# Performance work log

Hardware: AMD Instinct MI355X
Metric: run time of the kernel (lower is better)

## Reference

```python
import jax, jax.numpy as jnp
import numpy as np

B, IN, OUT = 8192, 1024, 1024


def setup_inputs() -> dict:
    key = jax.random.key(0)
    k1, k2 = jax.random.split(key)
    x = jax.random.normal(k1, (B, IN), dtype=jnp.float32)
    W_seed = jax.random.normal(k2, (IN, OUT), dtype=jnp.float32) / np.sqrt(IN).astype(np.float32)
    b_seed = jnp.zeros((OUT,), dtype=jnp.float32)
    W_sig = jnp.zeros((2,), dtype=jnp.float32)  # mixture logits over ['dense','Toeplitz']
    b_sig = jnp.zeros((2,), dtype=jnp.float32)  # mixture logits over ['dense','None']
    A_sig = jnp.zeros((2,), dtype=jnp.float32)  # mixture logits over ['linear','relu']
    return {"x": x, "W_seed": W_seed, "b_seed": b_seed,
            "W_sig": W_sig, "b_sig": b_sig, "A_sig": A_sig}


def _toeplitz_from_seed(W_seed):
    # seed_vec = [W_seed[0, out-1], ..., W_seed[0, 1], W_seed[0,0], ..., W_seed[in-1,0]]
    in_sz, out_sz = W_seed.shape
    seed_vec = jnp.concatenate([W_seed[0, -1:0:-1], W_seed[:, 0]])  # [out-1 + in]
    # W_toep[i, j] = seed_vec[i - j + out - 1]
    idx = jnp.arange(in_sz)[:, None] - jnp.arange(out_sz)[None, :] + (out_sz - 1)
    return seed_vec[idx]  # [in, out]


def reference(x, W_seed, b_seed, W_sig, b_sig, A_sig):
    W_toep = _toeplitz_from_seed(W_seed)
    w_s = jax.nn.softmax(W_sig)
    W_core = w_s[0] * W_seed + w_s[1] * W_toep          # softmax-weighted weight mixture
    b_s = jax.nn.softmax(b_sig)
    b_core = b_s[0] * b_seed                             # 'None' branch contributes zeros
    out = x @ W_core + b_core                            # [B, out]
    a_s = jax.nn.softmax(A_sig)
    return a_s[0] * out + a_s[1] * jax.nn.relu(out)      # activation mixture
```

## Files before the change

### kernel.cpp

```cpp
#include <hip/hip_runtime.h>

typedef unsigned short ushort_t;
typedef __bf16 bf16x8 __attribute__((ext_vector_type(8)));
typedef float f32x4 __attribute__((ext_vector_type(4)));

#define AS1 __attribute__((address_space(1)))
#define AS3 __attribute__((address_space(3)))

__device__ __forceinline__ ushort_t f2bf(float f) {
    unsigned u = __builtin_bit_cast(unsigned, f);
    u = (u + 0x7fffu + ((u >> 16) & 1u)) >> 16;
    return (ushort_t)u;
}

__device__ __forceinline__ void async16(void* lds, const void* g) {
    __builtin_amdgcn_global_load_lds((const AS1 unsigned int*)g,
                                     (AS3 unsigned int*)lds, 16, 0, 0);
}

__device__ __forceinline__ void softmax2(const float* __restrict__ sig, float& s0, float& s1) {
    float a = sig[0], b = sig[1];
    float m = fmaxf(a, b);
    float e0 = __expf(a - m), e1 = __expf(b - m);
    float inv = 1.0f / (e0 + e1);
    s0 = e0 * inv; s1 = e1 * inv;
}

__device__ __forceinline__ float toep_val(const float* __restrict__ Wseed, int k, int o) {
    return (k >= o) ? Wseed[(size_t)(k - o) << 10] : Wseed[o - k];
}

__global__ __launch_bounds__(256) void prep_kernel(const float* __restrict__ x,
                                                   const float* __restrict__ Wseed,
                                                   const float* __restrict__ Wsig,
                                                   ushort_t* __restrict__ xb,
                                                   ushort_t* __restrict__ Wt) {
    int b = blockIdx.x;
    if (b < 4096) {
        int i = b * 256 + threadIdx.x;
        const float4* xp = (const float4*)x + (size_t)i * 2;
        float4 a = xp[0], c = xp[1];
        uint4 r;
        r.x = (unsigned)f2bf(a.x) | ((unsigned)f2bf(a.y) << 16);
        r.y = (unsigned)f2bf(a.z) | ((unsigned)f2bf(a.w) << 16);
        r.z = (unsigned)f2bf(c.x) | ((unsigned)f2bf(c.y) << 16);
        r.w = (unsigned)f2bf(c.z) | ((unsigned)f2bf(c.w) << 16);
        ((uint4*)xb)[i] = r;
        return;
    }
    __shared__ float T[64][65];
    int bb = b - 4096;
    int k0 = (bb >> 4) * 64;
    int o0 = (bb & 15) * 64;
    int t = threadIdx.x;
    #pragma unroll
    for (int i = 0; i < 4; ++i) {
        int lin = t + i * 256;
        int kr = lin >> 4;
        int c4 = lin & 15;
        float4 v = *(const float4*)&Wseed[(size_t)(k0 + kr) * 1024 + o0 + c4 * 4];
        T[kr][c4 * 4 + 0] = v.x;
        T[kr][c4 * 4 + 1] = v.y;
        T[kr][c4 * 4 + 2] = v.z;
        T[kr][c4 * 4 + 3] = v.w;
    }
    __syncthreads();
    float s0, s1; softmax2(Wsig, s0, s1);
    #pragma unroll
    for (int i = 0; i < 2; ++i) {
        int lin = t + i * 256;
        int oo = lin >> 3;
        int kq = (lin & 7) * 8;
        unsigned r[4];
        #pragma unroll
        for (int q = 0; q < 4; ++q) {
            float v0 = s0 * T[kq + 2 * q + 0][oo] + s1 * toep_val(Wseed, k0 + kq + 2 * q + 0, o0 + oo);
            float v1 = s0 * T[kq + 2 * q + 1][oo] + s1 * toep_val(Wseed, k0 + kq + 2 * q + 1, o0 + oo);
            r[q] = (unsigned)f2bf(v0) | ((unsigned)f2bf(v1) << 16);
        }
        *(uint4*)&Wt[(size_t)(o0 + oo) * 1024 + k0 + kq] = make_uint4(r[0], r[1], r[2], r[3]);
    }
}

#define BM 128
#define BN 128
#define BK 64
#define NKT 16

__global__ __launch_bounds__(256, 2) void gemm_kernel(const ushort_t* __restrict__ Xb,
                                                      const ushort_t* __restrict__ Wt,
                                                      const float* __restrict__ bseed,
                                                      const float* __restrict__ bsig,
                                                      const float* __restrict__ asig,
                                                      float* __restrict__ out) {
    __shared__ ushort_t lds[32768];
    ushort_t* At0 = lds;
    ushort_t* Bt0 = lds + 8192;
    ushort_t* At1 = lds + 16384;
    ushort_t* Bt1 = lds + 24576;

    const int t = threadIdx.x;
    const int wv = t >> 6;
    const int lane = t & 63;

    const int orig = blockIdx.x;
    const int g = orig & 7;
    const int within = orig >> 3;
    const int rb = g * 8 + (within >> 3);
    const int cb = within & 7;
    const int brow = rb * BM;
    const int bcol = cb * BN;

    const int rs = t >> 3;
    const int cs = (t & 7) ^ (rs & 7);
    const ushort_t* gA = Xb + (size_t)(brow + rs) * 1024 + 8 * cs;
    const ushort_t* gB = Wt + (size_t)(bcol + rs) * 1024 + 8 * cs;

    f32x4 acc[4][4];
    #pragma unroll
    for (int i = 0; i < 4; ++i)
        #pragma unroll
        for (int j = 0; j < 4; ++j) acc[i][j] = (f32x4){0.f, 0.f, 0.f, 0.f};

    const int wr = (wv >> 1) * 64;
    const int wcn = (wv & 1) * 64;
    const int fr = lane & 15;
    const int kq = lane >> 4;

    float bs0, bs1, as0, as1;
    softmax2(bsig, bs0, bs1);
    softmax2(asig, as0, as1);
    float bias[4];
    #pragma unroll
    for (int ni = 0; ni < 4; ++ni)
        bias[ni] = bs0 * bseed[bcol + wcn + ni * 16 + fr];
    asm volatile("" :: "v"(bias[0]), "v"(bias[1]), "v"(bias[2]), "v"(bias[3]),
                       "v"(as0), "v"(as1));
    asm volatile("" ::: "memory");

#define STAGE1(buf, gptr, ko)                                      \
    do {                                                           \
        async16((buf) + wv * 512,        (gptr) + (ko));           \
        async16((buf) + 2048 + wv * 512, (gptr) + 32768 + (ko));   \
        async16((buf) + 4096 + wv * 512, (gptr) + 65536 + (ko));   \
        async16((buf) + 6144 + wv * 512, (gptr) + 98304 + (ko));   \
    } while (0)

#define STAGE(Abuf, Bbuf, ko) do { STAGE1(Abuf, gA, ko); STAGE1(Bbuf, gB, ko); } while (0)

#define COMPUTE(Abuf, Bbuf)                                                        \
    do {                                                                           \
        bf16x8 af[4][2], bf[4][2];                                                 \
        _Pragma("unroll")                                                          \
        for (int mi = 0; mi < 4; ++mi) {                                           \
            int row_ = wr + mi * 16 + fr;                                          \
            af[mi][0] = *(const bf16x8*)&(Abuf)[row_ * 64 + (((kq)     ^ (row_ & 7)) << 3)]; \
            af[mi][1] = *(const bf16x8*)&(Abuf)[row_ * 64 + (((kq + 4) ^ (row_ & 7)) << 3)]; \
        }                                                                          \
        _Pragma("unroll")                                                          \
        for (int ni = 0; ni < 4; ++ni) {                                           \
            int row_ = wcn + ni * 16 + fr;                                         \
            bf[ni][0] = *(const bf16x8*)&(Bbuf)[row_ * 64 + (((kq)     ^ (row_ & 7)) << 3)]; \
            bf[ni][1] = *(const bf16x8*)&(Bbuf)[row_ * 64 + (((kq + 4) ^ (row_ & 7)) << 3)]; \
        }                                                                          \
        _Pragma("unroll")                                                          \
        for (int mi = 0; mi < 4; ++mi)                                             \
            _Pragma("unroll")                                                      \
            for (int ni = 0; ni < 4; ++ni) {                                       \
                acc[mi][ni] = __builtin_amdgcn_mfma_f32_16x16x32_bf16(             \
                    af[mi][0], bf[ni][0], acc[mi][ni], 0, 0, 0);                   \
                acc[mi][ni] = __builtin_amdgcn_mfma_f32_16x16x32_bf16(             \
                    af[mi][1], bf[ni][1], acc[mi][ni], 0, 0, 0);                   \
            }                                                                      \
    } while (0)

#define SYNC() do { asm volatile("s_waitcnt vmcnt(0) lgkmcnt(0)" ::: "memory");    \
                    __builtin_amdgcn_s_barrier(); } while (0)

    STAGE(At0, Bt0, 0);
    SYNC();
    for (int it = 0; it < 7; ++it) {
        STAGE(At1, Bt1, (2 * it + 1) * BK);
        COMPUTE(At0, Bt0);
        SYNC();
        STAGE(At0, Bt0, (2 * it + 2) * BK);
        COMPUTE(At1, Bt1);
        SYNC();
    }
    STAGE(At1, Bt1, 15 * BK);
    COMPUTE(At0, Bt0);
    SYNC();
    COMPUTE(At1, Bt1);

    #pragma unroll
    for (int ni = 0; ni < 4; ++ni) {
        int col = bcol + wcn + ni * 16 + fr;
        #pragma unroll
        for (int mi = 0; mi < 4; ++mi) {
            int row = brow + wr + mi * 16 + (lane >> 4) * 4;
            #pragma unroll
            for (int r = 0; r < 4; ++r) {
                float v = acc[mi][ni][r] + bias[ni];
                out[(size_t)(row + r) * 1024 + col] = as0 * v + as1 * fmaxf(v, 0.f);
            }
        }
    }
#undef STAGE1
#undef STAGE
#undef COMPUTE
#undef SYNC
}

__global__ __launch_bounds__(256) void naive_kernel(const float* __restrict__ x,
                                                    const float* __restrict__ Wseed,
                                                    const float* __restrict__ bseed,
                                                    const float* __restrict__ Wsig,
                                                    const float* __restrict__ bsig,
                                                    const float* __restrict__ asig,
                                                    float* __restrict__ out) {
    int idx = blockIdx.x * 256 + threadIdx.x;
    int b = idx >> 10, o = idx & 1023;
    float ws0, ws1, bs0, bs1, as0, as1;
    softmax2(Wsig, ws0, ws1);
    softmax2(bsig, bs0, bs1);
    softmax2(asig, as0, as1);
    float s = 0.f;
    const float* xr = x + (size_t)b * 1024;
    for (int k = 0; k < 1024; ++k) {
        float wc = ws0 * Wseed[((size_t)k << 10) + o] + ws1 * toep_val(Wseed, k, o);
        s += xr[k] * wc;
    }
    float v = s + bs0 * bseed[o];
    out[idx] = as0 * v + as1 * fmaxf(v, 0.f);
}

extern "C" void kernel_launch(void* const* d_in, const int* in_sizes, int n_in,
                              void* d_out, int out_size, void* d_ws, size_t ws_size,
                              hipStream_t stream) {
    const float* x     = (const float*)d_in[0];
    const float* Wseed = (const float*)d_in[1];
    const float* bseed = (const float*)d_in[2];
    const float* Wsig  = (const float*)d_in[3];
    const float* bsig  = (const float*)d_in[4];
    const float* Asig  = (const float*)d_in[5];
    float* out = (float*)d_out;

    const size_t need = (2u << 20) + (16u << 20) + 1024;
    if (ws_size < need) {
        naive_kernel<<<dim3(8192 * 1024 / 256), dim3(256), 0, stream>>>(
            x, Wseed, bseed, Wsig, bsig, Asig, out);
        return;
    }

    ushort_t* Wt = (ushort_t*)d_ws;
    ushort_t* Xb = (ushort_t*)((char*)d_ws + (2u << 20));

    prep_kernel<<<dim3(4096 + 256), dim3(256), 0, stream>>>(x, Wseed, Wsig, Xb, Wt);
    gemm_kernel<<<dim3(512), dim3(256), 0, stream>>>(Xb, Wt, bseed, bsig, Asig, out);
}
```

Before: 39.45 us.

## Fuse fp32-to-bf16 conversion of x into GEMM A-tile loading

Drops the separate x-to-bf16 conversion pass and its 16MB workspace round trip. The GEMM now loads fp32 x tiles into registers one stage ahead, converts them to bf16 and writes them into swizzled LDS, while W tiles still use async global-to-LDS loads. Partial vmcnt waits let the register prefetch overlap with compute. The cost is more global bytes per A tile, more VGPR pressure from 16 prefetched float4 registers, and conversion work inside the main loop.

```diff
diff --git a/kernel.cpp b/kernel.cpp
--- a/kernel.cpp
+++ b/kernel.cpp
@@ -30,26 +30,11 @@
     return (k >= o) ? Wseed[(size_t)(k - o) << 10] : Wseed[o - k];
 }
 
-__global__ __launch_bounds__(256) void prep_kernel(const float* __restrict__ x,
-                                                   const float* __restrict__ Wseed,
-                                                   const float* __restrict__ Wsig,
-                                                   ushort_t* __restrict__ xb,
-                                                   ushort_t* __restrict__ Wt) {
-    int b = blockIdx.x;
-    if (b < 4096) {
-        int i = b * 256 + threadIdx.x;
-        const float4* xp = (const float4*)x + (size_t)i * 2;
-        float4 a = xp[0], c = xp[1];
-        uint4 r;
-        r.x = (unsigned)f2bf(a.x) | ((unsigned)f2bf(a.y) << 16);
-        r.y = (unsigned)f2bf(a.z) | ((unsigned)f2bf(a.w) << 16);
-        r.z = (unsigned)f2bf(c.x) | ((unsigned)f2bf(c.y) << 16);
-        r.w = (unsigned)f2bf(c.z) | ((unsigned)f2bf(c.w) << 16);
-        ((uint4*)xb)[i] = r;
-        return;
-    }
+__global__ __launch_bounds__(256) void prep_w_kernel(const float* __restrict__ Wseed,
+                                                     const float* __restrict__ Wsig,
+                                                     ushort_t* __restrict__ Wt) {
     __shared__ float T[64][65];
-    int bb = b - 4096;
+    int bb = blockIdx.x;
     int k0 = (bb >> 4) * 64;
     int o0 = (bb & 15) * 64;
     int t = threadIdx.x;
@@ -87,17 +72,17 @@
 #define BK 64
 #define NKT 16
 
-__global__ __launch_bounds__(256, 2) void gemm_kernel(const ushort_t* __restrict__ Xb,
+__global__ __launch_bounds__(256, 2) void gemm_kernel(const float* __restrict__ Xf,
                                                       const ushort_t* __restrict__ Wt,
                                                       const float* __restrict__ bseed,
                                                       const float* __restrict__ bsig,
                                                       const float* __restrict__ asig,
                                                       float* __restrict__ out) {
     __shared__ ushort_t lds[32768];
-    ushort_t* At0 = lds;
-    ushort_t* Bt0 = lds + 8192;
-    ushort_t* At1 = lds + 16384;
-    ushort_t* Bt1 = lds + 24576;
+    ushort_t* const A0buf = lds;
+    ushort_t* const A1buf = lds + 8192;
+    ushort_t* const B0buf = lds + 16384;
+    ushort_t* const B1buf = lds + 24576;
 
     const int t = threadIdx.x;
     const int wv = t >> 6;
@@ -113,19 +98,21 @@
 
     const int rs = t >> 3;
     const int cs = (t & 7) ^ (rs & 7);
-    const ushort_t* gA = Xb + (size_t)(brow + rs) * 1024 + 8 * cs;
     const ushort_t* gB = Wt + (size_t)(bcol + rs) * 1024 + 8 * cs;
 
-    f32x4 acc[4][4];
-    #pragma unroll
-    for (int i = 0; i < 4; ++i)
-        #pragma unroll
-        for (int j = 0; j < 4; ++j) acc[i][j] = (f32x4){0.f, 0.f, 0.f, 0.f};
+    const float* gX = Xf + (size_t)(brow + (t >> 3)) * 1024 + (t & 7) * 8;
+    const int wbase = (t >> 3) * 64 + (((t & 7) ^ ((t >> 3) & 7)) << 3);
 
     const int wr = (wv >> 1) * 64;
     const int wcn = (wv & 1) * 64;
     const int fr = lane & 15;
     const int kq = lane >> 4;
+
+    f32x4 acc[4][4];
+    #pragma unroll
+    for (int i = 0; i < 4; ++i)
+        #pragma unroll
+        for (int j = 0; j < 4; ++j) acc[i][j] = (f32x4){0.f, 0.f, 0.f, 0.f};
 
     float bs0, bs1, as0, as1;
     softmax2(bsig, bs0, bs1);
@@ -138,15 +125,47 @@
                        "v"(as0), "v"(as1));
     asm volatile("" ::: "memory");
 
-#define STAGE1(buf, gptr, ko)                                      \
-    do {                                                           \
-        async16((buf) + wv * 512,        (gptr) + (ko));           \
-        async16((buf) + 2048 + wv * 512, (gptr) + 32768 + (ko));   \
-        async16((buf) + 4096 + wv * 512, (gptr) + 65536 + (ko));   \
-        async16((buf) + 6144 + wv * 512, (gptr) + 98304 + (ko));   \
-    } while (0)
-
-#define STAGE(Abuf, Bbuf, ko) do { STAGE1(Abuf, gA, ko); STAGE1(Bbuf, gB, ko); } while (0)
+    f32x4 aE0, aE1, aE2, aE3, aE4, aE5, aE6, aE7;
+    f32x4 aO0, aO1, aO2, aO3, aO4, aO5, aO6, aO7;
+
+#define LOADA(P, ko)                                                   \
+    do {                                                               \
+        P##0 = *(const f32x4*)(gX + (ko));                             \
+        P##1 = *(const f32x4*)(gX + (ko) + 4);                         \
+        P##2 = *(const f32x4*)(gX + 32768 + (ko));                     \
+        P##3 = *(const f32x4*)(gX + 32768 + (ko) + 4);                 \
+        P##4 = *(const f32x4*)(gX + 65536 + (ko));                     \
+        P##5 = *(const f32x4*)(gX + 65536 + (ko) + 4);                 \
+        P##6 = *(const f32x4*)(gX + 98304 + (ko));                     \
+        P##7 = *(const f32x4*)(gX + 98304 + (ko) + 4);                 \
+    } while (0)
+
+#define CVW(Abuf, off, rlo, rhi)                                       \
+    do {                                                               \
+        bf16x8 v_;                                                     \
+        _Pragma("unroll")                                              \
+        for (int j_ = 0; j_ < 4; ++j_) {                               \
+            v_[j_]     = (__bf16)rlo[j_];                              \
+            v_[4 + j_] = (__bf16)rhi[j_];                              \
+        }                                                              \
+        *(bf16x8*)&(Abuf)[(off)] = v_;                                 \
+    } while (0)
+
+#define WRITEA(Abuf, P)                                                \
+    do {                                                               \
+        CVW(Abuf, wbase,        P##0, P##1);                           \
+        CVW(Abuf, wbase + 2048, P##2, P##3);                           \
+        CVW(Abuf, wbase + 4096, P##4, P##5);                           \
+        CVW(Abuf, wbase + 6144, P##6, P##7);                           \
+    } while (0)
+
+#define STAGEB(buf, ko)                                                \
+    do {                                                               \
+        async16((buf) + wv * 512,        gB + (ko));                   \
+        async16((buf) + 2048 + wv * 512, gB + 32768 + (ko));           \
+        async16((buf) + 4096 + wv * 512, gB + 65536 + (ko));           \
+        async16((buf) + 6144 + wv * 512, gB + 98304 + (ko));           \
+    } while (0)
 
 #define COMPUTE(Abuf, Bbuf)                                                        \
     do {                                                                           \
@@ -174,23 +193,38 @@
             }                                                                      \
     } while (0)
 
-#define SYNC() do { asm volatile("s_waitcnt vmcnt(0) lgkmcnt(0)" ::: "memory");    \
-                    __builtin_amdgcn_s_barrier(); } while (0)
-
-    STAGE(At0, Bt0, 0);
-    SYNC();
-    for (int it = 0; it < 7; ++it) {
-        STAGE(At1, Bt1, (2 * it + 1) * BK);
-        COMPUTE(At0, Bt0);
-        SYNC();
-        STAGE(At0, Bt0, (2 * it + 2) * BK);
-        COMPUTE(At1, Bt1);
-        SYNC();
-    }
-    STAGE(At1, Bt1, 15 * BK);
-    COMPUTE(At0, Bt0);
-    SYNC();
-    COMPUTE(At1, Bt1);
+#define ENDSYNC8() do { asm volatile("" ::: "memory");                               \
+                        asm volatile("s_waitcnt vmcnt(8)" ::: "memory");             \
+                        asm volatile("s_waitcnt lgkmcnt(0)" ::: "memory");           \
+                        __builtin_amdgcn_s_barrier(); } while (0)
+#define ENDSYNC0() do { asm volatile("" ::: "memory");                               \
+                        asm volatile("s_waitcnt vmcnt(0) lgkmcnt(0)" ::: "memory");  \
+                        __builtin_amdgcn_s_barrier(); } while (0)
+
+    LOADA(aE, 0);
+    STAGEB(B0buf, 0);
+    LOADA(aO, 64);
+    WRITEA(A0buf, aE);
+    ENDSYNC8();
+
+    for (int i = 0; i < 7; ++i) {
+        const int T = 2 * i;
+        STAGEB(B1buf, (size_t)(T + 1) * BK);
+        LOADA(aE, (size_t)(T + 2) * BK);
+        WRITEA(A1buf, aO);
+        COMPUTE(A0buf, B0buf);
+        ENDSYNC8();
+        STAGEB(B0buf, (size_t)(T + 2) * BK);
+        LOADA(aO, (size_t)(T + 3) * BK);
+        WRITEA(A0buf, aE);
+        COMPUTE(A1buf, B1buf);
+        ENDSYNC8();
+    }
+    STAGEB(B1buf, 15 * BK);
+    WRITEA(A1buf, aO);
+    COMPUTE(A0buf, B0buf);
+    ENDSYNC0();
+    COMPUTE(A1buf, B1buf);
 
     #pragma unroll
     for (int ni = 0; ni < 4; ++ni) {
@@ -205,10 +239,13 @@
             }
         }
     }
-#undef STAGE1
-#undef STAGE
+#undef LOADA
+#undef CVW
+#undef WRITEA
+#undef STAGEB
 #undef COMPUTE
-#undef SYNC
+#undef ENDSYNC8
+#undef ENDSYNC0
 }
 
 __global__ __launch_bounds__(256) void naive_kernel(const float* __restrict__ x,
@@ -245,7 +282,7 @@
     const float* Asig  = (const float*)d_in[5];
     float* out = (float*)d_out;
 
-    const size_t need = (2u << 20) + (16u << 20) + 1024;
+    const size_t need = (2u << 20) + 1024;
     if (ws_size < need) {
         naive_kernel<<<dim3(8192 * 1024 / 256), dim3(256), 0, stream>>>(
             x, Wseed, bseed, Wsig, bsig, Asig, out);
@@ -253,8 +290,7 @@
     }
 
     ushort_t* Wt = (ushort_t*)d_ws;
-    ushort_t* Xb = (ushort_t*)((char*)d_ws + (2u << 20));
-
-    prep_kernel<<<dim3(4096 + 256), dim3(256), 0, stream>>>(x, Wseed, Wsig, Xb, Wt);
-    gemm_kernel<<<dim3(512), dim3(256), 0, stream>>>(Xb, Wt, bseed, bsig, Asig, out);
-}
+
+    prep_w_kernel<<<dim3(256), dim3(256), 0, stream>>>(Wseed, Wsig, Wt);
+    gemm_kernel<<<dim3(512), dim3(256), 0, stream>>>(x, Wt, bseed, bsig, Asig, out);
+}
```

After: 37.03 us. 6.1% less time.
